# Performance work log

Hardware: AMD Instinct MI355X
Metric: run time of the kernel (lower is better)

Reference implementation:

```python
import jax, jax.numpy as jnp
import numpy as np

N_USERS = 50000
N_ITEMS = 10000
N_ENTITIES = 40000
N_NODES = N_USERS + N_ITEMS + N_ENTITIES  # 100000
EMB = 64
NNZ = 1600000  # avg degree 16
VIS_DIM = 2048
TXT_DIM = 300


def setup_inputs() -> dict:
    key = jax.random.key(0)
    ks = jax.random.split(key, 16)
    def xn(k, shape, scale=0.05):
        return jax.random.normal(k, shape, dtype=jnp.float32) * scale
    return {
        "adj_row": jax.random.randint(ks[0], (NNZ,), 0, N_NODES, dtype=jnp.int32),
        "adj_col": jax.random.randint(ks[1], (NNZ,), 0, N_NODES, dtype=jnp.int32),
        "adj_val": jax.random.uniform(ks[2], (NNZ,), dtype=jnp.float32) / 16.0,  # ~normalized adj
        "embedding": xn(ks[3], (N_NODES, EMB), 0.1),
        "visual_features": jax.random.normal(ks[4], (N_ITEMS, VIS_DIM), dtype=jnp.float32),
        "text_features": jax.random.normal(ks[5], (N_ITEMS, TXT_DIM), dtype=jnp.float32),
        "Wv1": xn(ks[6], (512, VIS_DIM)), "bv1": jnp.zeros((512,), jnp.float32),
        "Wv2": xn(ks[7], (EMB, 512)),    "bv2": jnp.zeros((EMB,), jnp.float32),
        "Wt1": xn(ks[8], (256, TXT_DIM)), "bt1": jnp.zeros((256,), jnp.float32),
        "Wt2": xn(ks[9], (EMB, 256)),    "bt2": jnp.zeros((EMB,), jnp.float32),
        "Wd": xn(ks[10], (EMB, EMB)),    "bd": jnp.zeros((EMB,), jnp.float32),
        "Wc0": xn(ks[11], (EMB, 2 * EMB)), "bc0": jnp.zeros((EMB,), jnp.float32),
        "Wc1": xn(ks[12], (EMB, 2 * EMB)), "bc1": jnp.zeros((EMB,), jnp.float32),
    }


def _lin(x, W, b):
    return x @ W.T + b


def reference(adj_row, adj_col, adj_val, embedding, visual_features, text_features,
              Wv1, bv1, Wv2, bv2, Wt1, bt1, Wt2, bt2, Wd, bd, Wc0, bc0, Wc1, bc1):
    # multimodal item encoding (eval mode: dropout = identity)
    vis = _lin(jax.nn.relu(_lin(visual_features, Wv1, bv1)), Wv2, bv2)
    vis = _lin(vis, Wd, bd)
    txt = _lin(jax.nn.relu(_lin(text_features, Wt1, bt1)), Wt2, bt2)
    txt = _lin(txt, Wd, bd)
    fused_item = (vis + txt) * 0.5  # [n_items, emb]

    ego = embedding.at[N_USERS:N_USERS + N_ITEMS].set(fused_item)

    all_embs = [ego]
    cur = ego
    for Wc, bc in ((Wc0, bc0), (Wc1, bc1)):
        # SpMM: neighbor[i] = sum_j A[i,j] * cur[j]
        msgs = adj_val[:, None] * cur[adj_col]            # [nnz, emb]
        nb = jax.ops.segment_sum(msgs, adj_row, num_segments=N_NODES)
        cur = _lin(jnp.concatenate([cur, nb], axis=-1), Wc, bc)  # W_concat
        cur = jax.nn.leaky_relu(cur, 0.01)                # F.leaky_relu default slope
        all_embs.append(cur)

    return jnp.concatenate(all_embs, axis=-1)  # [n_nodes, emb*(n_layers+1)]
```

## Files before the change

kernel.cpp:

```cpp
#include <hip/hip_runtime.h>
#include <hip/hip_bf16.h>
#include <cstddef>

#define N_USERS 50000
#define N_ITEMS 10000
#define N_NODES 100000
#define EMB 64
#define NNZ_E 1600000
#define VIS_DIM 2048
#define TXT_DIM 300

typedef short bf16x8 __attribute__((ext_vector_type(8)));
typedef float f32x4  __attribute__((ext_vector_type(4)));

__device__ inline unsigned short f2bf(float x) {
    __hip_bfloat16 h = __float2bfloat16(x);
    return __builtin_bit_cast(unsigned short, h);
}
__device__ inline float bf2f(unsigned short u) {
    unsigned int t = ((unsigned int)u) << 16;
    float f;
    __builtin_memcpy(&f, &t, 4);
    return f;
}

#define GLDW 40

__global__ __launch_bounds__(256, 2) void gemm_bf3(
    const float* __restrict__ A, const float* __restrict__ W,
    const float* __restrict__ bias, float* __restrict__ C,
    int M, int N, int K, int relu)
{
    __shared__ unsigned short Ah[128][GLDW], Al[128][GLDW];
    __shared__ unsigned short Wh[128][GLDW], Wl[128][GLDW];

    const int t   = threadIdx.x;
    const int w   = t >> 6;
    const int l   = t & 63;
    const int l16 = l & 15;
    const int lq  = l >> 4;
    const int m0  = blockIdx.y * 128;
    const int n0  = blockIdx.x * 128;
    const int mh  = (w & 1) * 64;
    const int nh  = (w >> 1) * 64;

    const int r0 = t >> 2,          kc0 = t & 3;
    const int r1 = (t + 256) >> 2,  kc1 = t & 3;

    f32x4 acc[4][4] = {};

    const int kiters = (K + 31) / 32;

    float pa[2][8], pw[2][8];

    {
        const int k0 = 0;
        #pragma unroll
        for (int p = 0; p < 2; p++) {
            int row = p ? r1 : r0, kc = p ? kc1 : kc0;
            int rg = m0 + row; if (rg >= M) rg = M - 1;
            const float* g = A + (size_t)rg * K + k0 + kc * 8;
            if (k0 + kc * 8 + 7 < K) {
                float4 q0 = *(const float4*)g, q1 = *(const float4*)(g + 4);
                pa[p][0]=q0.x; pa[p][1]=q0.y; pa[p][2]=q0.z; pa[p][3]=q0.w;
                pa[p][4]=q1.x; pa[p][5]=q1.y; pa[p][6]=q1.z; pa[p][7]=q1.w;
            } else {
                #pragma unroll
                for (int i = 0; i < 8; i++)
                    pa[p][i] = (k0 + kc * 8 + i < K) ? g[i] : 0.f;
            }
            int ng = n0 + row; if (ng >= N) ng = N - 1;
            const float* gw = W + (size_t)ng * K + k0 + kc * 8;
            if (k0 + kc * 8 + 7 < K) {
                float4 q0 = *(const float4*)gw, q1 = *(const float4*)(gw + 4);
                pw[p][0]=q0.x; pw[p][1]=q0.y; pw[p][2]=q0.z; pw[p][3]=q0.w;
                pw[p][4]=q1.x; pw[p][5]=q1.y; pw[p][6]=q1.z; pw[p][7]=q1.w;
            } else {
                #pragma unroll
                for (int i = 0; i < 8; i++)
                    pw[p][i] = (k0 + kc * 8 + i < K) ? gw[i] : 0.f;
            }
        }
    }

    for (int kt = 0; kt < kiters; kt++) {
        #pragma unroll
        for (int p = 0; p < 2; p++) {
            int row = p ? r1 : r0, kc = p ? kc1 : kc0;
            bf16x8 hi, lo;
            #pragma unroll
            for (int i = 0; i < 8; i++) {
                unsigned short h = f2bf(pa[p][i]);
                hi[i] = (short)h;
                lo[i] = (short)f2bf(pa[p][i] - bf2f(h));
            }
            *(bf16x8*)&Ah[row][kc * 8] = hi;
            *(bf16x8*)&Al[row][kc * 8] = lo;
            #pragma unroll
            for (int i = 0; i < 8; i++) {
                unsigned short h = f2bf(pw[p][i]);
                hi[i] = (short)h;
                lo[i] = (short)f2bf(pw[p][i] - bf2f(h));
            }
            *(bf16x8*)&Wh[row][kc * 8] = hi;
            *(bf16x8*)&Wl[row][kc * 8] = lo;
        }
        __syncthreads();

        if (kt + 1 < kiters) {
            const int k0 = (kt + 1) * 32;
            #pragma unroll
            for (int p = 0; p < 2; p++) {
                int row = p ? r1 : r0, kc = p ? kc1 : kc0;
                int rg = m0 + row; if (rg >= M) rg = M - 1;
                const float* g = A + (size_t)rg * K + k0 + kc * 8;
                if (k0 + kc * 8 + 7 < K) {
                    float4 q0 = *(const float4*)g, q1 = *(const float4*)(g + 4);
                    pa[p][0]=q0.x; pa[p][1]=q0.y; pa[p][2]=q0.z; pa[p][3]=q0.w;
                    pa[p][4]=q1.x; pa[p][5]=q1.y; pa[p][6]=q1.z; pa[p][7]=q1.w;
                } else {
                    #pragma unroll
                    for (int i = 0; i < 8; i++)
                        pa[p][i] = (k0 + kc * 8 + i < K) ? g[i] : 0.f;
                }
                int ng = n0 + row; if (ng >= N) ng = N - 1;
                const float* gw = W + (size_t)ng * K + k0 + kc * 8;
                if (k0 + kc * 8 + 7 < K) {
                    float4 q0 = *(const float4*)gw, q1 = *(const float4*)(gw + 4);
                    pw[p][0]=q0.x; pw[p][1]=q0.y; pw[p][2]=q0.z; pw[p][3]=q0.w;
                    pw[p][4]=q1.x; pw[p][5]=q1.y; pw[p][6]=q1.z; pw[p][7]=q1.w;
                } else {
                    #pragma unroll
                    for (int i = 0; i < 8; i++)
                        pw[p][i] = (k0 + kc * 8 + i < K) ? gw[i] : 0.f;
                }
            }
        }

        {
            bf16x8 ah[4], al[4];
            #pragma unroll
            for (int mi = 0; mi < 4; mi++) {
                ah[mi] = *(const bf16x8*)&Ah[mh + mi * 16 + l16][lq * 8];
                al[mi] = *(const bf16x8*)&Al[mh + mi * 16 + l16][lq * 8];
            }
            #pragma unroll
            for (int ni = 0; ni < 4; ni++) {
                bf16x8 bh = *(const bf16x8*)&Wh[nh + ni * 16 + l16][lq * 8];
                bf16x8 bl = *(const bf16x8*)&Wl[nh + ni * 16 + l16][lq * 8];
                #pragma unroll
                for (int mi = 0; mi < 4; mi++) {
                    acc[mi][ni] = __builtin_amdgcn_mfma_f32_16x16x32_bf16(
                        ah[mi], bh, acc[mi][ni], 0, 0, 0);
                    acc[mi][ni] = __builtin_amdgcn_mfma_f32_16x16x32_bf16(
                        ah[mi], bl, acc[mi][ni], 0, 0, 0);
                    acc[mi][ni] = __builtin_amdgcn_mfma_f32_16x16x32_bf16(
                        al[mi], bh, acc[mi][ni], 0, 0, 0);
                }
            }
        }
        __syncthreads();
    }

    #pragma unroll
    for (int ni = 0; ni < 4; ni++) {
        int col = n0 + nh + ni * 16 + l16;
        float bcol = bias[col];
        #pragma unroll
        for (int mi = 0; mi < 4; mi++) {
            #pragma unroll
            for (int r = 0; r < 4; r++) {
                int row = m0 + mh + mi * 16 + lq * 4 + r;
                if (row >= M) continue;
                float v = acc[mi][ni][r] + bcol;
                if (relu) v = fmaxf(v, 0.f);
                C[(size_t)row * N + col] = v;
            }
        }
    }
}

__global__ __launch_bounds__(256, 2) void concat_mfma(
    const float* __restrict__ cur, const float* __restrict__ nbuf,
    const float* __restrict__ Wc, const float* __restrict__ bias,
    float* __restrict__ out_cur, float* __restrict__ out_full, int col_off)
{
    __shared__ unsigned short Ah[128][GLDW], Al[128][GLDW];
    __shared__ unsigned short Bh[64][GLDW],  Bl[64][GLDW];

    const int t   = threadIdx.x;
    const int w   = t >> 6;
    const int l   = t & 63;
    const int l16 = l & 15;
    const int lq  = l >> 4;
    const int m0  = blockIdx.x * 128;
    const int mh  = w * 32;

    const int r  = t >> 2;
    const int kc = t & 3;

    f32x4 acc[2][4] = {};

    float pa[2][8], pw[8];

    auto load_tile = [&](int kt) {
        const float* src = (kt < 2) ? cur : nbuf;
        const int kcol = (kt & 1) * 32 + kc * 8;
        #pragma unroll
        for (int p = 0; p < 2; p++) {
            int rg = m0 + r + p * 64;
            if (rg >= N_NODES) rg = N_NODES - 1;
            const float* g = src + (size_t)rg * 64 + kcol;
            float4 q0 = *(const float4*)g, q1 = *(const float4*)(g + 4);
            pa[p][0]=q0.x; pa[p][1]=q0.y; pa[p][2]=q0.z; pa[p][3]=q0.w;
            pa[p][4]=q1.x; pa[p][5]=q1.y; pa[p][6]=q1.z; pa[p][7]=q1.w;
        }
        const float* gw = Wc + (size_t)r * 128 + kt * 32 + kc * 8;
        float4 q0 = *(const float4*)gw, q1 = *(const float4*)(gw + 4);
        pw[0]=q0.x; pw[1]=q0.y; pw[2]=q0.z; pw[3]=q0.w;
        pw[4]=q1.x; pw[5]=q1.y; pw[6]=q1.z; pw[7]=q1.w;
    };

    load_tile(0);

    for (int kt = 0; kt < 4; kt++) {
        #pragma unroll
        for (int p = 0; p < 2; p++) {
            bf16x8 hi, lo;
            #pragma unroll
            for (int i = 0; i < 8; i++) {
                unsigned short h = f2bf(pa[p][i]);
                hi[i] = (short)h;
                lo[i] = (short)f2bf(pa[p][i] - bf2f(h));
            }
            *(bf16x8*)&Ah[r + p * 64][kc * 8] = hi;
            *(bf16x8*)&Al[r + p * 64][kc * 8] = lo;
        }
        {
            bf16x8 hi, lo;
            #pragma unroll
            for (int i = 0; i < 8; i++) {
                unsigned short h = f2bf(pw[i]);
                hi[i] = (short)h;
                lo[i] = (short)f2bf(pw[i] - bf2f(h));
            }
            *(bf16x8*)&Bh[r][kc * 8] = hi;
            *(bf16x8*)&Bl[r][kc * 8] = lo;
        }
        __syncthreads();

        if (kt < 3) load_tile(kt + 1);

        {
            bf16x8 ah[2], al[2];
            #pragma unroll
            for (int mi = 0; mi < 2; mi++) {
                ah[mi] = *(const bf16x8*)&Ah[mh + mi * 16 + l16][lq * 8];
                al[mi] = *(const bf16x8*)&Al[mh + mi * 16 + l16][lq * 8];
            }
            #pragma unroll
            for (int ni = 0; ni < 4; ni++) {
                bf16x8 bh = *(const bf16x8*)&Bh[ni * 16 + l16][lq * 8];
                bf16x8 bl = *(const bf16x8*)&Bl[ni * 16 + l16][lq * 8];
                #pragma unroll
                for (int mi = 0; mi < 2; mi++) {
                    acc[mi][ni] = __builtin_amdgcn_mfma_f32_16x16x32_bf16(
                        ah[mi], bh, acc[mi][ni], 0, 0, 0);
                    acc[mi][ni] = __builtin_amdgcn_mfma_f32_16x16x32_bf16(
                        ah[mi], bl, acc[mi][ni], 0, 0, 0);
                    acc[mi][ni] = __builtin_amdgcn_mfma_f32_16x16x32_bf16(
                        al[mi], bh, acc[mi][ni], 0, 0, 0);
                }
            }
        }
        __syncthreads();
    }

    #pragma unroll
    for (int ni = 0; ni < 4; ni++) {
        int col = ni * 16 + l16;
        float bcol = bias[col];
        #pragma unroll
        for (int mi = 0; mi < 2; mi++) {
            #pragma unroll
            for (int rr = 0; rr < 4; rr++) {
                int row = m0 + mh + mi * 16 + lq * 4 + rr;
                if (row >= N_NODES) continue;
                float v = acc[mi][ni][rr] + bcol;
                v = (v > 0.f) ? v : 0.01f * v;
                if (out_cur) out_cur[(size_t)row * 64 + col] = v;
                out_full[(size_t)row * 192 + col_off + col] = v;
            }
        }
    }
}

__global__ void transp64(const float* __restrict__ W, float* __restrict__ wT, int K)
{
    int i = blockIdx.x * 256 + threadIdx.x;
    if (i >= 64 * K) return;
    int d = i / K, k = i - d * K;
    wT[k * 64 + d] = W[i];
}

__global__ __launch_bounds__(256) void linear64(
    const float* __restrict__ in, const float* __restrict__ wT,
    const float* __restrict__ bias, float* __restrict__ out,
    int M, int K, float in_scale, int add)
{
    int t  = threadIdx.x;
    int d  = t & 63;
    int w  = t >> 6;
    int m0 = blockIdx.x * 16 + w * 4;
    if (m0 >= M) return;
    int mlast = M - 1;
    int m1 = (m0 + 1 < M) ? m0 + 1 : mlast;
    int m2 = (m0 + 2 < M) ? m0 + 2 : mlast;
    int m3 = (m0 + 3 < M) ? m0 + 3 : mlast;

    const float* x0 = in + (size_t)m0 * K;
    const float* x1 = in + (size_t)m1 * K;
    const float* x2 = in + (size_t)m2 * K;
    const float* x3 = in + (size_t)m3 * K;

    float a0 = 0.f, a1 = 0.f, a2 = 0.f, a3 = 0.f;

    for (int k = 0; k < K; k += 8) {
        const float* wp = wT + (size_t)k * 64 + d;
        float w0 = wp[0],   w1 = wp[64],  w2 = wp[128], w3 = wp[192];
        float w4 = wp[256], w5 = wp[320], w6 = wp[384], w7 = wp[448];
        float4 p0 = *(const float4*)(x0 + k), q0 = *(const float4*)(x0 + k + 4);
        float4 p1 = *(const float4*)(x1 + k), q1 = *(const float4*)(x1 + k + 4);
        float4 p2 = *(const float4*)(x2 + k), q2 = *(const float4*)(x2 + k + 4);
        float4 p3 = *(const float4*)(x3 + k), q3 = *(const float4*)(x3 + k + 4);
        a0 += p0.x*w0 + p0.y*w1 + p0.z*w2 + p0.w*w3
            + q0.x*w4 + q0.y*w5 + q0.z*w6 + q0.w*w7;
        a1 += p1.x*w0 + p1.y*w1 + p1.z*w2 + p1.w*w3
            + q1.x*w4 + q1.y*w5 + q1.z*w6 + q1.w*w7;
        a2 += p2.x*w0 + p2.y*w1 + p2.z*w2 + p2.w*w3
            + q2.x*w4 + q2.y*w5 + q2.z*w6 + q2.w*w7;
        a3 += p3.x*w0 + p3.y*w1 + p3.z*w2 + p3.w*w3
            + q3.x*w4 + q3.y*w5 + q3.z*w6 + q3.w*w7;
    }

    float b = bias[d];
    float r0 = a0 * in_scale + b;
    float r1 = a1 * in_scale + b;
    float r2 = a2 * in_scale + b;
    float r3 = a3 * in_scale + b;
    if (add) {
        out[(size_t)m0 * 64 + d] += r0;
        if (m0 + 1 < M) out[(size_t)m1 * 64 + d] += r1;
        if (m0 + 2 < M) out[(size_t)m2 * 64 + d] += r2;
        if (m0 + 3 < M) out[(size_t)m3 * 64 + d] += r3;
    } else {
        out[(size_t)m0 * 64 + d] = r0;
        if (m0 + 1 < M) out[(size_t)m1 * 64 + d] = r1;
        if (m0 + 2 < M) out[(size_t)m2 * 64 + d] = r2;
        if (m0 + 3 < M) out[(size_t)m3 * 64 + d] = r3;
    }
}

__global__ void ego_fill(const float* __restrict__ emb, float* __restrict__ cur0,
                         float* __restrict__ out_full)
{
    int tid = blockIdx.x * 256 + threadIdx.x;
    if (tid >= N_NODES * EMB) return;
    int m = tid >> 6, d = tid & 63;
    float v;
    if (m < N_USERS || m >= N_USERS + N_ITEMS) {
        v = emb[tid];
        cur0[tid] = v;
    } else {
        v = cur0[tid];
    }
    out_full[(size_t)m * 192 + d] = v;
}

__global__ __launch_bounds__(256) void hist_rows(
    const int* __restrict__ row, int* __restrict__ cnt, int nnz)
{
    int e = blockIdx.x * 256 + threadIdx.x;
    if (e >= nnz) return;
    atomicAdd(&cnt[row[e]], 1);
}

__global__ __launch_bounds__(256) void scan1(int* __restrict__ cnt,
                                             int* __restrict__ bsum, int n)
{
    __shared__ int part[256];
    int t = threadIdx.x;
    int base = blockIdx.x * 1024 + t * 4;
    int v0 = 0, v1 = 0, v2 = 0, v3 = 0;
    if (base + 0 < n) v0 = cnt[base + 0];
    if (base + 1 < n) v1 = cnt[base + 1];
    if (base + 2 < n) v2 = cnt[base + 2];
    if (base + 3 < n) v3 = cnt[base + 3];
    int s = v0 + v1 + v2 + v3;
    part[t] = s;
    __syncthreads();
    for (int off = 1; off < 256; off <<= 1) {
        int x = (t >= off) ? part[t - off] : 0;
        __syncthreads();
        part[t] += x;
        __syncthreads();
    }
    int excl = part[t] - s;
    if (t == 255) bsum[blockIdx.x] = part[t];
    if (base + 0 < n) cnt[base + 0] = excl;
    if (base + 1 < n) cnt[base + 1] = excl + v0;
    if (base + 2 < n) cnt[base + 2] = excl + v0 + v1;
    if (base + 3 < n) cnt[base + 3] = excl + v0 + v1 + v2;
}

__global__ void scan2(int* __restrict__ bsum, int nb)
{
    if (threadIdx.x == 0 && blockIdx.x == 0) {
        int acc = 0;
        for (int i = 0; i < nb; i++) { int v = bsum[i]; bsum[i] = acc; acc += v; }
    }
}

__global__ __launch_bounds__(256) void scan3(
    const int* __restrict__ excl, const int* __restrict__ bsum,
    int* __restrict__ row_ptr, int* __restrict__ row_cur, int n, int nnz)
{
    int i = blockIdx.x * 256 + threadIdx.x;
    if (i > n) return;
    if (i == n) { row_ptr[n] = nnz; return; }
    int v = excl[i] + bsum[i >> 10];
    row_ptr[i] = v;
    row_cur[i] = v;
}

__global__ __launch_bounds__(256) void scatter_csr(
    const int* __restrict__ row, const int* __restrict__ col,
    const float* __restrict__ val, int* __restrict__ row_cur,
    int* __restrict__ col_s, float* __restrict__ val_s, int nnz)
{
    int e = blockIdx.x * 256 + threadIdx.x;
    if (e >= nnz) return;
    int r = row[e];
    int p = atomicAdd(&row_cur[r], 1);
    col_s[p] = col[e];
    val_s[p] = val[e];
}

__global__ __launch_bounds__(256) void spmm_gather(
    const int* __restrict__ row_ptr, const int* __restrict__ col_s,
    const float* __restrict__ val_s, const float* __restrict__ cur,
    float* __restrict__ nb)
{
    int t  = threadIdx.x;
    int wv = t >> 6;
    int l  = t & 63;
    int eg = l >> 4;
    int dg = l & 15;
    int m = blockIdx.x * 4 + wv;
    if (m >= N_NODES) return;
    int beg = row_ptr[m], end = row_ptr[m + 1];
    float ax = 0.f, ay = 0.f, az = 0.f, aw = 0.f;
    for (int j = beg + eg; j < end; j += 4) {
        int   c = col_s[j];
        float v = val_s[j];
        float4 cv = *(const float4*)&cur[(size_t)c * 64 + dg * 4];
        ax += v * cv.x; ay += v * cv.y; az += v * cv.z; aw += v * cv.w;
    }
    ax += __shfl_xor(ax, 16, 64); ay += __shfl_xor(ay, 16, 64);
    az += __shfl_xor(az, 16, 64); aw += __shfl_xor(aw, 16, 64);
    ax += __shfl_xor(ax, 32, 64); ay += __shfl_xor(ay, 32, 64);
    az += __shfl_xor(az, 32, 64); aw += __shfl_xor(aw, 32, 64);
    if (eg == 0) {
        float4 r; r.x = ax; r.y = ay; r.z = az; r.w = aw;
        *(float4*)&nb[(size_t)m * 64 + dg * 4] = r;
    }
}

extern "C" void kernel_launch(void* const* d_in, const int* in_sizes, int n_in,
                              void* d_out, int out_size, void* d_ws, size_t ws_size,
                              hipStream_t stream)
{
    const int*   adj_row = (const int*)  d_in[0];
    const int*   adj_col = (const int*)  d_in[1];
    const float* adj_val = (const float*)d_in[2];
    const float* emb     = (const float*)d_in[3];
    const float* visf    = (const float*)d_in[4];
    const float* txtf    = (const float*)d_in[5];
    const float* Wv1 = (const float*)d_in[6];  const float* bv1 = (const float*)d_in[7];
    const float* Wv2 = (const float*)d_in[8];  const float* bv2 = (const float*)d_in[9];
    const float* Wt1 = (const float*)d_in[10]; const float* bt1 = (const float*)d_in[11];
    const float* Wt2 = (const float*)d_in[12]; const float* bt2 = (const float*)d_in[13];
    const float* Wd  = (const float*)d_in[14]; const float* bd  = (const float*)d_in[15];
    const float* Wc0 = (const float*)d_in[16]; const float* bc0 = (const float*)d_in[17];
    const float* Wc1 = (const float*)d_in[18]; const float* bc1 = (const float*)d_in[19];

    float* out = (float*)d_out;
    float* ws  = (float*)d_ws;

    float* H1v  = ws + 0;
    float* H1t  = ws + 5120000;
    float* nb   = ws + 0;
    float* s    = ws + 7680000;
    float* cur0 = ws + 8320000;
    float* cur1 = ws + 14720000;
    float* wv2T = ws + 21120000;
    float* wt2T = wv2T + 32768;
    float* wdT  = wt2T + 16384;
    int*   col_s   = (int*)  (ws + 21200000);
    float* val_s   =          ws + 22800000;
    int*   row_ptr = (int*)  (ws + 24400000);
    int*   row_cur = (int*)  (ws + 24510000);
    int*   cnt     = (int*)  (ws + 24620000);
    int*   bsum    = (int*)  (ws + 24730000);

    const int NBLK = (N_NODES + 1023) / 1024;

    transp64<<<(64 * 512 + 255) / 256, 256, 0, stream>>>(Wv2, wv2T, 512);
    transp64<<<(64 * 256 + 255) / 256, 256, 0, stream>>>(Wt2, wt2T, 256);
    transp64<<<(64 * 64  + 255) / 256, 256, 0, stream>>>(Wd,  wdT,  64);

    hipMemsetAsync(cnt, 0, N_NODES * sizeof(int), stream);
    hist_rows<<<(NNZ_E + 255) / 256, 256, 0, stream>>>(adj_row, cnt, NNZ_E);
    scan1<<<NBLK, 256, 0, stream>>>(cnt, bsum, N_NODES);
    scan2<<<1, 64, 0, stream>>>(bsum, NBLK);
    scan3<<<(N_NODES + 256) / 256, 256, 0, stream>>>(cnt, bsum, row_ptr, row_cur,
                                                     N_NODES, NNZ_E);
    scatter_csr<<<(NNZ_E + 255) / 256, 256, 0, stream>>>(adj_row, adj_col, adj_val,
                                                         row_cur, col_s, val_s, NNZ_E);

    {
        dim3 g(512 / 128, (N_ITEMS + 127) / 128);
        gemm_bf3<<<g, 256, 0, stream>>>(visf, Wv1, bv1, H1v, N_ITEMS, 512, VIS_DIM, 1);
    }
    {
        dim3 g(256 / 128, (N_ITEMS + 127) / 128);
        gemm_bf3<<<g, 256, 0, stream>>>(txtf, Wt1, bt1, H1t, N_ITEMS, 256, TXT_DIM, 1);
    }

    linear64<<<(N_ITEMS + 15) / 16, 256, 0, stream>>>(H1v, wv2T, bv2, s, N_ITEMS, 512, 1.0f, 0);
    linear64<<<(N_ITEMS + 15) / 16, 256, 0, stream>>>(H1t, wt2T, bt2, s, N_ITEMS, 256, 1.0f, 1);
    linear64<<<(N_ITEMS + 15) / 16, 256, 0, stream>>>(s, wdT, bd, cur0 + (size_t)N_USERS * 64,
                                                      N_ITEMS, 64, 0.5f, 0);

    ego_fill<<<(N_NODES * EMB + 255) / 256, 256, 0, stream>>>(emb, cur0, out);

    spmm_gather<<<(N_NODES + 3) / 4, 256, 0, stream>>>(row_ptr, col_s, val_s, cur0, nb);
    concat_mfma<<<(N_NODES + 127) / 128, 256, 0, stream>>>(cur0, nb, Wc0, bc0, cur1, out, 64);

    spmm_gather<<<(N_NODES + 3) / 4, 256, 0, stream>>>(row_ptr, col_s, val_s, cur1, nb);
    concat_mfma<<<(N_NODES + 127) / 128, 256, 0, stream>>>(cur1, nb, Wc1, bc1, nullptr, out, 128);
}
```

Before: 797.0 us.

## Replace LDS-tiled GEMM with direct-global split-K MFMA GEMM, fuse ReLU into linear

Swaps the shared-memory tiled bf16x3 GEMM for a templated kernel in which each wave loads its A and W fragments straight from global memory, with no LDS and no barriers. The visual GEMM is split over K into two planes whose partial sums are added and passed through ReLU inside the following linear64 kernel. The text GEMM uses smaller 32x32 wave tiles to launch more blocks. This aims to raise parallelism on the 10000x512x2048 GEMM and drop LDS synchronisation, at the cost of redundant global loads across waves, an extra partial buffer written and read, and a larger read in linear64.

```diff
diff --git a/kernel.cpp b/kernel.cpp
--- a/kernel.cpp
+++ b/kernel.cpp
@@ -24,161 +24,124 @@
     return f;
 }
 
-#define GLDW 40
-
-__global__ __launch_bounds__(256, 2) void gemm_bf3(
+template<int MI, int NI>
+__global__ __launch_bounds__(256) void gemm_dg(
     const float* __restrict__ A, const float* __restrict__ W,
     const float* __restrict__ bias, float* __restrict__ C,
-    int M, int N, int K, int relu)
-{
-    __shared__ unsigned short Ah[128][GLDW], Al[128][GLDW];
-    __shared__ unsigned short Wh[128][GLDW], Wl[128][GLDW];
-
+    int M, int N, int K, int k_per, long long c_plane,
+    int act, int add_bias)
+{
     const int t   = threadIdx.x;
     const int w   = t >> 6;
     const int l   = t & 63;
     const int l16 = l & 15;
     const int lq  = l >> 4;
-    const int m0  = blockIdx.y * 128;
-    const int n0  = blockIdx.x * 128;
-    const int mh  = (w & 1) * 64;
-    const int nh  = (w >> 1) * 64;
-
-    const int r0 = t >> 2,          kc0 = t & 3;
-    const int r1 = (t + 256) >> 2,  kc1 = t & 3;
-
-    f32x4 acc[4][4] = {};
-
-    const int kiters = (K + 31) / 32;
-
-    float pa[2][8], pw[2][8];
-
-    {
-        const int k0 = 0;
-        #pragma unroll
-        for (int p = 0; p < 2; p++) {
-            int row = p ? r1 : r0, kc = p ? kc1 : kc0;
-            int rg = m0 + row; if (rg >= M) rg = M - 1;
-            const float* g = A + (size_t)rg * K + k0 + kc * 8;
-            if (k0 + kc * 8 + 7 < K) {
-                float4 q0 = *(const float4*)g, q1 = *(const float4*)(g + 4);
-                pa[p][0]=q0.x; pa[p][1]=q0.y; pa[p][2]=q0.z; pa[p][3]=q0.w;
-                pa[p][4]=q1.x; pa[p][5]=q1.y; pa[p][6]=q1.z; pa[p][7]=q1.w;
+
+    const int n0 = blockIdx.x * (NI * 16);
+    const int m0 = (blockIdx.y * 4 + w) * (MI * 16);
+    if (m0 >= M) return;
+    const int kz = blockIdx.z;
+    const int kb = kz * k_per;
+    int krem = K - kb; if (krem > k_per) krem = k_per;
+    const int kiters = (krem + 31) / 32;
+    float* Cz = C + (long long)kz * c_plane;
+
+    const float* ap[MI];
+    #pragma unroll
+    for (int mi = 0; mi < MI; mi++) {
+        int r = m0 + mi * 16 + l16; if (r >= M) r = M - 1;
+        ap[mi] = A + (size_t)r * K;
+    }
+    const float* wpt[NI];
+    #pragma unroll
+    for (int ni = 0; ni < NI; ni++) {
+        int r = n0 + ni * 16 + l16; if (r >= N) r = N - 1;
+        wpt[ni] = W + (size_t)r * K;
+    }
+
+    f32x4 acc[MI][NI] = {};
+
+    for (int kt = 0; kt < kiters; kt++) {
+        const int k0 = kb + kt * 32 + lq * 8;
+
+        bf16x8 ahi[MI], alo[MI];
+        #pragma unroll
+        for (int mi = 0; mi < MI; mi++) {
+            float v[8];
+            if (k0 + 7 < K) {
+                float4 q0 = *(const float4*)(ap[mi] + k0);
+                float4 q1 = *(const float4*)(ap[mi] + k0 + 4);
+                v[0]=q0.x; v[1]=q0.y; v[2]=q0.z; v[3]=q0.w;
+                v[4]=q1.x; v[5]=q1.y; v[6]=q1.z; v[7]=q1.w;
             } else {
                 #pragma unroll
                 for (int i = 0; i < 8; i++)
-                    pa[p][i] = (k0 + kc * 8 + i < K) ? g[i] : 0.f;
-            }
-            int ng = n0 + row; if (ng >= N) ng = N - 1;
-            const float* gw = W + (size_t)ng * K + k0 + kc * 8;
-            if (k0 + kc * 8 + 7 < K) {
-                float4 q0 = *(const float4*)gw, q1 = *(const float4*)(gw + 4);
-                pw[p][0]=q0.x; pw[p][1]=q0.y; pw[p][2]=q0.z; pw[p][3]=q0.w;
-                pw[p][4]=q1.x; pw[p][5]=q1.y; pw[p][6]=q1.z; pw[p][7]=q1.w;
+                    v[i] = (k0 + i < K) ? ap[mi][k0 + i] : 0.f;
+            }
+            #pragma unroll
+            for (int i = 0; i < 8; i++) {
+                unsigned short h = f2bf(v[i]);
+                ahi[mi][i] = (short)h;
+                alo[mi][i] = (short)f2bf(v[i] - bf2f(h));
+            }
+        }
+
+        bf16x8 whi[NI], wlo[NI];
+        #pragma unroll
+        for (int ni = 0; ni < NI; ni++) {
+            float v[8];
+            if (k0 + 7 < K) {
+                float4 q0 = *(const float4*)(wpt[ni] + k0);
+                float4 q1 = *(const float4*)(wpt[ni] + k0 + 4);
+                v[0]=q0.x; v[1]=q0.y; v[2]=q0.z; v[3]=q0.w;
+                v[4]=q1.x; v[5]=q1.y; v[6]=q1.z; v[7]=q1.w;
             } else {
                 #pragma unroll
                 for (int i = 0; i < 8; i++)
-                    pw[p][i] = (k0 + kc * 8 + i < K) ? gw[i] : 0.f;
-            }
-        }
-    }
-
-    for (int kt = 0; kt < kiters; kt++) {
-        #pragma unroll
-        for (int p = 0; p < 2; p++) {
-            int row = p ? r1 : r0, kc = p ? kc1 : kc0;
-            bf16x8 hi, lo;
+                    v[i] = (k0 + i < K) ? wpt[ni][k0 + i] : 0.f;
+            }
             #pragma unroll
             for (int i = 0; i < 8; i++) {
-                unsigned short h = f2bf(pa[p][i]);
-                hi[i] = (short)h;
-                lo[i] = (short)f2bf(pa[p][i] - bf2f(h));
-            }
-            *(bf16x8*)&Ah[row][kc * 8] = hi;
-            *(bf16x8*)&Al[row][kc * 8] = lo;
-            #pragma unroll
-            for (int i = 0; i < 8; i++) {
-                unsigned short h = f2bf(pw[p][i]);
-                hi[i] = (short)h;
-                lo[i] = (short)f2bf(pw[p][i] - bf2f(h));
-            }
-            *(bf16x8*)&Wh[row][kc * 8] = hi;
-            *(bf16x8*)&Wl[row][kc * 8] = lo;
-        }
-        __syncthreads();
-
-        if (kt + 1 < kiters) {
-            const int k0 = (kt + 1) * 32;
-            #pragma unroll
-            for (int p = 0; p < 2; p++) {
-                int row = p ? r1 : r0, kc = p ? kc1 : kc0;
-                int rg = m0 + row; if (rg >= M) rg = M - 1;
-                const float* g = A + (size_t)rg * K + k0 + kc * 8;
-                if (k0 + kc * 8 + 7 < K) {
-                    float4 q0 = *(const float4*)g, q1 = *(const float4*)(g + 4);
-                    pa[p][0]=q0.x; pa[p][1]=q0.y; pa[p][2]=q0.z; pa[p][3]=q0.w;
-                    pa[p][4]=q1.x; pa[p][5]=q1.y; pa[p][6]=q1.z; pa[p][7]=q1.w;
-                } else {
-                    #pragma unroll
-                    for (int i = 0; i < 8; i++)
-                        pa[p][i] = (k0 + kc * 8 + i < K) ? g[i] : 0.f;
-                }
-                int ng = n0 + row; if (ng >= N) ng = N - 1;
-                const float* gw = W + (size_t)ng * K + k0 + kc * 8;
-                if (k0 + kc * 8 + 7 < K) {
-                    float4 q0 = *(const float4*)gw, q1 = *(const float4*)(gw + 4);
-                    pw[p][0]=q0.x; pw[p][1]=q0.y; pw[p][2]=q0.z; pw[p][3]=q0.w;
-                    pw[p][4]=q1.x; pw[p][5]=q1.y; pw[p][6]=q1.z; pw[p][7]=q1.w;
-                } else {
-                    #pragma unroll
-                    for (int i = 0; i < 8; i++)
-                        pw[p][i] = (k0 + kc * 8 + i < K) ? gw[i] : 0.f;
-                }
-            }
-        }
-
-        {
-            bf16x8 ah[4], al[4];
-            #pragma unroll
-            for (int mi = 0; mi < 4; mi++) {
-                ah[mi] = *(const bf16x8*)&Ah[mh + mi * 16 + l16][lq * 8];
-                al[mi] = *(const bf16x8*)&Al[mh + mi * 16 + l16][lq * 8];
-            }
-            #pragma unroll
-            for (int ni = 0; ni < 4; ni++) {
-                bf16x8 bh = *(const bf16x8*)&Wh[nh + ni * 16 + l16][lq * 8];
-                bf16x8 bl = *(const bf16x8*)&Wl[nh + ni * 16 + l16][lq * 8];
-                #pragma unroll
-                for (int mi = 0; mi < 4; mi++) {
-                    acc[mi][ni] = __builtin_amdgcn_mfma_f32_16x16x32_bf16(
-                        ah[mi], bh, acc[mi][ni], 0, 0, 0);
-                    acc[mi][ni] = __builtin_amdgcn_mfma_f32_16x16x32_bf16(
-                        ah[mi], bl, acc[mi][ni], 0, 0, 0);
-                    acc[mi][ni] = __builtin_amdgcn_mfma_f32_16x16x32_bf16(
-                        al[mi], bh, acc[mi][ni], 0, 0, 0);
-                }
-            }
-        }
-        __syncthreads();
+                unsigned short h = f2bf(v[i]);
+                whi[ni][i] = (short)h;
+                wlo[ni][i] = (short)f2bf(v[i] - bf2f(h));
+            }
+        }
+
+        #pragma unroll
+        for (int ni = 0; ni < NI; ni++) {
+            #pragma unroll
+            for (int mi = 0; mi < MI; mi++) {
+                acc[mi][ni] = __builtin_amdgcn_mfma_f32_16x16x32_bf16(
+                    ahi[mi], whi[ni], acc[mi][ni], 0, 0, 0);
+                acc[mi][ni] = __builtin_amdgcn_mfma_f32_16x16x32_bf16(
+                    ahi[mi], wlo[ni], acc[mi][ni], 0, 0, 0);
+                acc[mi][ni] = __builtin_amdgcn_mfma_f32_16x16x32_bf16(
+                    alo[mi], whi[ni], acc[mi][ni], 0, 0, 0);
+            }
+        }
     }
 
     #pragma unroll
-    for (int ni = 0; ni < 4; ni++) {
-        int col = n0 + nh + ni * 16 + l16;
-        float bcol = bias[col];
-        #pragma unroll
-        for (int mi = 0; mi < 4; mi++) {
+    for (int ni = 0; ni < NI; ni++) {
+        int col = n0 + ni * 16 + l16;
+        if (col >= N) continue;
+        float b = (add_bias && kz == 0) ? bias[col] : 0.f;
+        #pragma unroll
+        for (int mi = 0; mi < MI; mi++) {
             #pragma unroll
             for (int r = 0; r < 4; r++) {
-                int row = m0 + mh + mi * 16 + lq * 4 + r;
+                int row = m0 + mi * 16 + lq * 4 + r;
                 if (row >= M) continue;
-                float v = acc[mi][ni][r] + bcol;
-                if (relu) v = fmaxf(v, 0.f);
-                C[(size_t)row * N + col] = v;
-            }
-        }
-    }
-}
+                float vv = acc[mi][ni][r] + b;
+                if (act) vv = fmaxf(vv, 0.f);
+                Cz[(size_t)row * N + col] = vv;
+            }
+        }
+    }
+}
+
+#define GLDW 40
 
 __global__ __launch_bounds__(256, 2) void concat_mfma(
     const float* __restrict__ cur, const float* __restrict__ nbuf,
@@ -304,9 +267,10 @@
 }
 
 __global__ __launch_bounds__(256) void linear64(
-    const float* __restrict__ in, const float* __restrict__ wT,
-    const float* __restrict__ bias, float* __restrict__ out,
-    int M, int K, float in_scale, int add)
+    const float* __restrict__ in, const float* __restrict__ in2,
+    const float* __restrict__ wT, const float* __restrict__ bias,
+    float* __restrict__ out, int M, int K, float in_scale, int add,
+    int fuse_relu)
 {
     int t  = threadIdx.x;
     int d  = t & 63;
@@ -322,6 +286,10 @@
     const float* x1 = in + (size_t)m1 * K;
     const float* x2 = in + (size_t)m2 * K;
     const float* x3 = in + (size_t)m3 * K;
+    const float* y0 = fuse_relu ? in2 + (size_t)m0 * K : x0;
+    const float* y1 = fuse_relu ? in2 + (size_t)m1 * K : x1;
+    const float* y2 = fuse_relu ? in2 + (size_t)m2 * K : x2;
+    const float* y3 = fuse_relu ? in2 + (size_t)m3 * K : x3;
 
     float a0 = 0.f, a1 = 0.f, a2 = 0.f, a3 = 0.f;
 
@@ -333,6 +301,28 @@
         float4 p1 = *(const float4*)(x1 + k), q1 = *(const float4*)(x1 + k + 4);
         float4 p2 = *(const float4*)(x2 + k), q2 = *(const float4*)(x2 + k + 4);
         float4 p3 = *(const float4*)(x3 + k), q3 = *(const float4*)(x3 + k + 4);
+        if (fuse_relu) {
+            float4 r0 = *(const float4*)(y0 + k), s0 = *(const float4*)(y0 + k + 4);
+            float4 r1 = *(const float4*)(y1 + k), s1 = *(const float4*)(y1 + k + 4);
+            float4 r2 = *(const float4*)(y2 + k), s2 = *(const float4*)(y2 + k + 4);
+            float4 r3 = *(const float4*)(y3 + k), s3 = *(const float4*)(y3 + k + 4);
+            p0.x=fmaxf(p0.x+r0.x,0.f); p0.y=fmaxf(p0.y+r0.y,0.f);
+            p0.z=fmaxf(p0.z+r0.z,0.f); p0.w=fmaxf(p0.w+r0.w,0.f);
+            q0.x=fmaxf(q0.x+s0.x,0.f); q0.y=fmaxf(q0.y+s0.y,0.f);
+            q0.z=fmaxf(q0.z+s0.z,0.f); q0.w=fmaxf(q0.w+s0.w,0.f);
+            p1.x=fmaxf(p1.x+r1.x,0.f); p1.y=fmaxf(p1.y+r1.y,0.f);
+            p1.z=fmaxf(p1.z+r1.z,0.f); p1.w=fmaxf(p1.w+r1.w,0.f);
+            q1.x=fmaxf(q1.x+s1.x,0.f); q1.y=fmaxf(q1.y+s1.y,0.f);
+            q1.z=fmaxf(q1.z+s1.z,0.f); q1.w=fmaxf(q1.w+s1.w,0.f);
+            p2.x=fmaxf(p2.x+r2.x,0.f); p2.y=fmaxf(p2.y+r2.y,0.f);
+            p2.z=fmaxf(p2.z+r2.z,0.f); p2.w=fmaxf(p2.w+r2.w,0.f);
+            q2.x=fmaxf(q2.x+s2.x,0.f); q2.y=fmaxf(q2.y+s2.y,0.f);
+            q2.z=fmaxf(q2.z+s2.z,0.f); q2.w=fmaxf(q2.w+s2.w,0.f);
+            p3.x=fmaxf(p3.x+r3.x,0.f); p3.y=fmaxf(p3.y+r3.y,0.f);
+            p3.z=fmaxf(p3.z+r3.z,0.f); p3.w=fmaxf(p3.w+r3.w,0.f);
+            q3.x=fmaxf(q3.x+s3.x,0.f); q3.y=fmaxf(q3.y+s3.y,0.f);
+            q3.z=fmaxf(q3.z+s3.z,0.f); q3.w=fmaxf(q3.w+s3.w,0.f);
+        }
         a0 += p0.x*w0 + p0.y*w1 + p0.z*w2 + p0.w*w3
             + q0.x*w4 + q0.y*w5 + q0.z*w6 + q0.w*w7;
         a1 += p1.x*w0 + p1.y*w1 + p1.z*w2 + p1.w*w3
@@ -503,6 +493,7 @@
     float* s    = ws + 7680000;
     float* cur0 = ws + 8320000;
     float* cur1 = ws + 14720000;
+    float* H1v2 = ws + 14720000;
     float* wv2T = ws + 21120000;
     float* wt2T = wv2T + 32768;
     float* wdT  = wt2T + 16384;
@@ -529,18 +520,26 @@
                                                          row_cur, col_s, val_s, NNZ_E);
 
     {
-        dim3 g(512 / 128, (N_ITEMS + 127) / 128);
-        gemm_bf3<<<g, 256, 0, stream>>>(visf, Wv1, bv1, H1v, N_ITEMS, 512, VIS_DIM, 1);
+        dim3 g(512 / 64, (157 + 3) / 4, 2);
+        gemm_dg<4, 4><<<g, 256, 0, stream>>>(visf, Wv1, bv1, H1v,
+                                             N_ITEMS, 512, VIS_DIM,
+                                             1024, (long long)14720000,
+                                             0, 1);
     }
     {
-        dim3 g(256 / 128, (N_ITEMS + 127) / 128);
-        gemm_bf3<<<g, 256, 0, stream>>>(txtf, Wt1, bt1, H1t, N_ITEMS, 256, TXT_DIM, 1);
-    }
-
-    linear64<<<(N_ITEMS + 15) / 16, 256, 0, stream>>>(H1v, wv2T, bv2, s, N_ITEMS, 512, 1.0f, 0);
-    linear64<<<(N_ITEMS + 15) / 16, 256, 0, stream>>>(H1t, wt2T, bt2, s, N_ITEMS, 256, 1.0f, 1);
-    linear64<<<(N_ITEMS + 15) / 16, 256, 0, stream>>>(s, wdT, bd, cur0 + (size_t)N_USERS * 64,
-                                                      N_ITEMS, 64, 0.5f, 0);
+        dim3 g(256 / 32, (313 + 3) / 4, 1);
+        gemm_dg<2, 2><<<g, 256, 0, stream>>>(txtf, Wt1, bt1, H1t,
+                                             N_ITEMS, 256, TXT_DIM,
+                                             512, 0, 1, 1);
+    }
+
+    linear64<<<(N_ITEMS + 15) / 16, 256, 0, stream>>>(H1v, H1v2, wv2T, bv2, s,
+                                                      N_ITEMS, 512, 1.0f, 0, 1);
+    linear64<<<(N_ITEMS + 15) / 16, 256, 0, stream>>>(H1t, nullptr, wt2T, bt2, s,
+                                                      N_ITEMS, 256, 1.0f, 1, 0);
+    linear64<<<(N_ITEMS + 15) / 16, 256, 0, stream>>>(s, nullptr, wdT, bd,
+                                                      cur0 + (size_t)N_USERS * 64,
+                                                      N_ITEMS, 64, 0.5f, 0, 0);
 
     ego_fill<<<(N_NODES * EMB + 255) / 256, 256, 0, stream>>>(emb, cur0, out);
 
```

Measured after the change: 987.1 us. 23.9% more time.
